# Optimization experiments

Hardware: AMD Instinct MI355X
Metric: run time of the kernel (lower is better)

The kernel has to match this reference:

```python
import jax, jax.numpy as jnp
import numpy as np

N_NODES = 50000
N_EDGES = 800000
IN_HID = 64
OUT_HID = 64
EXT_DIM = 32


def setup_inputs() -> dict:
    key = jax.random.key(0)
    ks = jax.random.split(key, 9)
    h = jax.random.normal(ks[0], (N_NODES, IN_HID), dtype=jnp.float32)
    e_h = jax.random.normal(ks[1], (N_EDGES, IN_HID), dtype=jnp.float32)
    ext_feature = jax.random.normal(ks[2], (N_EDGES, EXT_DIM), dtype=jnp.float32)
    # fc1: Linear(3*in_hid -> in_hid); fc2: Linear(in_hid+ext_dim -> out_hid)
    W1 = jax.random.normal(ks[3], (3 * IN_HID, IN_HID), dtype=jnp.float32) * 0.05
    b1 = jax.random.normal(ks[4], (IN_HID,), dtype=jnp.float32) * 0.05
    W2 = jax.random.normal(ks[5], (IN_HID + EXT_DIM, OUT_HID), dtype=jnp.float32) * 0.05
    b2 = jax.random.normal(ks[6], (OUT_HID,), dtype=jnp.float32) * 0.05
    src = jax.random.randint(ks[7], (N_EDGES,), 0, N_NODES, dtype=jnp.int64 if jax.config.jax_enable_x64 else jnp.int32)
    dst = jax.random.randint(ks[8], (N_EDGES,), 0, N_NODES, dtype=jnp.int64 if jax.config.jax_enable_x64 else jnp.int32)
    return {"h": h, "e_h": e_h, "ext_feature": ext_feature,
            "W1": W1, "b1": b1, "W2": W2, "b2": b2,
            "src": src, "dst": dst}


def reference(h, e_h, ext_feature, W1, b1, W2, b2, src, dst):
    # apply_edge: gather src/dst node features, concat with edge feature
    evt = jnp.concatenate([h[src], e_h, h[dst]], axis=-1)          # [E, 3*in_hid]
    x = evt @ W1 + b1                                              # fc1 (dropout=0 -> identity)
    x = jnp.concatenate([x, ext_feature], axis=-1)                 # [E, in_hid+ext_dim]
    out = jax.nn.relu(x @ W2 + b2)                                 # fc2 + relu; activation=None
    return out                                                     # new edge feature e_h [E, out_hid]
```

## Files before the change

### kernel.cpp

```cpp
#include <hip/hip_runtime.h>


typedef __attribute__((ext_vector_type(8))) short bf16x8;
typedef __attribute__((ext_vector_type(4))) float f32x4;

__device__ __forceinline__ short f2bf(float f) {
  unsigned u = __builtin_bit_cast(unsigned, f);
  u = (u + 0x7FFFu + ((u >> 16) & 1u)) >> 16;
  return (short)u;
}


__global__ __launch_bounds__(256, 2) void edge_mp_kernel(
    const float* __restrict__ h, const float* __restrict__ e_h,
    const float* __restrict__ ext, const float* __restrict__ W1,
    const float* __restrict__ b1, const float* __restrict__ W2,
    const float* __restrict__ b2, const int* __restrict__ src,
    const int* __restrict__ dst, float* __restrict__ out, int E) {
  __shared__ __align__(16) short lds[30720];
  const int tid = threadIdx.x;
  const int l = tid & 63;
  const int wid = tid >> 6;
  const int i = l & 15;
  const int q = l >> 4;
  const int i2 = l >> 2;
  const int c = l & 3;

  for (int s = tid; s < 1536; s += 256) {
    int kc = s >> 8, nt = (s >> 6) & 3, ll = s & 63;
    int k0 = kc * 32 + ((ll >> 4) * 8), n = nt * 16 + (ll & 15);
#pragma unroll
    for (int j = 0; j < 8; ++j) lds[s * 8 + j] = f2bf(W1[(k0 + j) * 64 + n]);
  }
  for (int s = tid; s < 768; s += 256) {
    int kc = s >> 8, nt = (s >> 6) & 3, ll = s & 63;
    int k0 = kc * 32 + ((ll >> 4) * 8), n = nt * 16 + (ll & 15);
#pragma unroll
    for (int j = 0; j < 8; ++j)
      lds[12288 + s * 8 + j] = f2bf(W2[(k0 + j) * 64 + n]);
  }
  __syncthreads();

  float b1v[4], b2v[4];
#pragma unroll
  for (int nt = 0; nt < 4; ++nt) {
    b1v[nt] = b1[nt * 16 + i];
    b2v[nt] = b2[nt * 16 + i];
  }

  short* evt = &lds[18432 + wid * 3072];

  for (int it = 0; it < 4; ++it) {
    const int e0 = blockIdx.x * 256 + it * 64 + wid * 16;
    if (e0 >= E) break;
    int e = e0 + i2;
    if (e >= E) e = E - 1;
    const int sI = src[e], dI = dst[e];
    const float* srcp[3] = {h + (size_t)sI * 64, e_h + (size_t)e * 64,
                            h + (size_t)dI * 64};

#pragma unroll
    for (int s = 0; s < 3; ++s) {
#pragma unroll
      for (int t = 0; t < 4; ++t) {
        const int k0 = 16 * t + 4 * c;
        float4 v = *(const float4*)(srcp[s] + k0);
        const int kc = s * 2 + (t >> 1);
        const int quad = 2 * (t & 1) + (c >> 1);
        const int j0 = 4 * (c & 1);
        short4 p;
        p.x = f2bf(v.x); p.y = f2bf(v.y); p.z = f2bf(v.z); p.w = f2bf(v.w);
        *(short4*)&evt[(kc * 64 + quad * 16 + i2) * 8 + j0] = p;
      }
    }

    f32x4 acc[4] = {{0.f, 0.f, 0.f, 0.f},
                    {0.f, 0.f, 0.f, 0.f},
                    {0.f, 0.f, 0.f, 0.f},
                    {0.f, 0.f, 0.f, 0.f}};
#pragma unroll
    for (int kc = 0; kc < 6; ++kc) {
      bf16x8 a = *(const bf16x8*)&evt[(kc * 64 + l) * 8];
#pragma unroll
      for (int nt = 0; nt < 4; ++nt) {
        bf16x8 b = *(const bf16x8*)&lds[((kc * 4 + nt) * 64 + l) * 8];
        acc[nt] = __builtin_amdgcn_mfma_f32_16x16x32_bf16(a, b, acc[nt], 0, 0, 0);
      }
    }

#pragma unroll
    for (int nt = 0; nt < 4; ++nt) {
      const int n = nt * 16 + i;
      const int kc2 = n >> 5, qA = (n & 31) >> 3, j = n & 7;
#pragma unroll
      for (int r = 0; r < 4; ++r) {
        const int m = q * 4 + r;
        evt[(kc2 * 64 + qA * 16 + m) * 8 + j] = f2bf(acc[nt][r] + b1v[nt]);
      }
    }
#pragma unroll
    for (int t = 0; t < 2; ++t) {
      float4 v = *(const float4*)(ext + (size_t)e * 32 + 16 * t + 4 * c);
      const int quad = 2 * t + (c >> 1);
      const int j0 = 4 * (c & 1);
      short4 p;
      p.x = f2bf(v.x); p.y = f2bf(v.y); p.z = f2bf(v.z); p.w = f2bf(v.w);
      *(short4*)&evt[(2 * 64 + quad * 16 + i2) * 8 + j0] = p;
    }

    f32x4 acc2[4] = {{0.f, 0.f, 0.f, 0.f},
                     {0.f, 0.f, 0.f, 0.f},
                     {0.f, 0.f, 0.f, 0.f},
                     {0.f, 0.f, 0.f, 0.f}};
#pragma unroll
    for (int kc = 0; kc < 3; ++kc) {
      bf16x8 a = *(const bf16x8*)&evt[(kc * 64 + l) * 8];
#pragma unroll
      for (int nt = 0; nt < 4; ++nt) {
        bf16x8 b = *(const bf16x8*)&lds[12288 + ((kc * 4 + nt) * 64 + l) * 8];
        acc2[nt] =
            __builtin_amdgcn_mfma_f32_16x16x32_bf16(a, b, acc2[nt], 0, 0, 0);
      }
    }

#pragma unroll
    for (int nt = 0; nt < 4; ++nt) {
      const int n = nt * 16 + i;
#pragma unroll
      for (int r = 0; r < 4; ++r) {
        const int er = e0 + q * 4 + r;
        if (er < E) {
          float v = acc2[nt][r] + b2v[nt];
          out[(size_t)er * 64 + n] = fmaxf(v, 0.f);
        }
      }
    }
  }
}

extern "C" void kernel_launch(void* const* d_in, const int* in_sizes, int n_in,
                              void* d_out, int out_size, void* d_ws,
                              size_t ws_size, hipStream_t stream) {
  const float* h = (const float*)d_in[0];
  const float* e_h = (const float*)d_in[1];
  const float* ext = (const float*)d_in[2];
  const float* W1 = (const float*)d_in[3];
  const float* b1 = (const float*)d_in[4];
  const float* W2 = (const float*)d_in[5];
  const float* b2 = (const float*)d_in[6];
  const int* src = (const int*)d_in[7];
  const int* dst = (const int*)d_in[8];
  float* out = (float*)d_out;
  const int E = in_sizes[7];
  const int blocks = (E + 255) / 256;
  hipLaunchKernelGGL(edge_mp_kernel, dim3(blocks), dim3(256), 0, stream, h, e_h,
                     ext, W1, b1, W2, b2, src, dst, out, E);
}
```

Before: 457.4 us.

## Load gathered features straight into MFMA A registers and prefetch edge indices

The fc1 A operand is now built directly in registers. Each lane loads the 16-row by 32-k slice that matches the MFMA operand layout from the src, edge and dst feature rows, so the per-wave LDS staging buffer for the 192-wide concat is gone and only the fc2 input is staged. Next iteration's src/dst indices are prefetched and the ext loads are issued early to hide gather latency. Blocks grow to 512 threads with launch_bounds(512,4). That launch bound squeezes registers against the twelve float4 held per lane, which risks spilling or lower occupancy.

```diff
diff --git a/kernel.cpp b/kernel.cpp
--- a/kernel.cpp
+++ b/kernel.cpp
@@ -3,6 +3,7 @@
 
 typedef __attribute__((ext_vector_type(8))) short bf16x8;
 typedef __attribute__((ext_vector_type(4))) float f32x4;
+typedef __attribute__((ext_vector_type(4))) short s16x4;
 
 __device__ __forceinline__ short f2bf(float f) {
   unsigned u = __builtin_bit_cast(unsigned, f);
@@ -10,8 +11,10 @@
   return (short)u;
 }
 
+#define ITERS 4
 
-__global__ __launch_bounds__(256, 2) void edge_mp_kernel(
+
+__global__ __launch_bounds__(512, 4) void edge_mp_kernel(
     const float* __restrict__ h, const float* __restrict__ e_h,
     const float* __restrict__ ext, const float* __restrict__ W1,
     const float* __restrict__ b1, const float* __restrict__ W2,
@@ -26,13 +29,13 @@
   const int i2 = l >> 2;
   const int c = l & 3;
 
-  for (int s = tid; s < 1536; s += 256) {
+  for (int s = tid; s < 1536; s += 512) {
     int kc = s >> 8, nt = (s >> 6) & 3, ll = s & 63;
     int k0 = kc * 32 + ((ll >> 4) * 8), n = nt * 16 + (ll & 15);
 #pragma unroll
     for (int j = 0; j < 8; ++j) lds[s * 8 + j] = f2bf(W1[(k0 + j) * 64 + n]);
   }
-  for (int s = tid; s < 768; s += 256) {
+  for (int s = tid; s < 768; s += 512) {
     int kc = s >> 8, nt = (s >> 6) & 3, ll = s & 63;
     int k0 = kc * 32 + ((ll >> 4) * 8), n = nt * 16 + (ll & 15);
 #pragma unroll
@@ -48,29 +51,54 @@
     b2v[nt] = b2[nt * 16 + i];
   }
 
-  short* evt = &lds[18432 + wid * 3072];
+  short* xw = &lds[18432 + wid * 1536];
 
-  for (int it = 0; it < 4; ++it) {
-    const int e0 = blockIdx.x * 256 + it * 64 + wid * 16;
+  const int base = blockIdx.x * (128 * ITERS) + wid * 16;
+
+  int nS = 0, nD = 0;
+  if (base < E) {
+    int e = base + i;
+    if (e >= E) e = E - 1;
+    nS = src[e];
+    nD = dst[e];
+  }
+
+#pragma unroll 1
+  for (int it = 0; it < ITERS; ++it) {
+    const int e0 = base + it * 128;
     if (e0 >= E) break;
-    int e = e0 + i2;
+    int e = e0 + i;
     if (e >= E) e = E - 1;
-    const int sI = src[e], dI = dst[e];
-    const float* srcp[3] = {h + (size_t)sI * 64, e_h + (size_t)e * 64,
-                            h + (size_t)dI * 64};
 
-#pragma unroll
-    for (int s = 0; s < 3; ++s) {
-#pragma unroll
-      for (int t = 0; t < 4; ++t) {
-        const int k0 = 16 * t + 4 * c;
-        float4 v = *(const float4*)(srcp[s] + k0);
-        const int kc = s * 2 + (t >> 1);
-        const int quad = 2 * (t & 1) + (c >> 1);
-        const int j0 = 4 * (c & 1);
-        short4 p;
-        p.x = f2bf(v.x); p.y = f2bf(v.y); p.z = f2bf(v.z); p.w = f2bf(v.w);
-        *(short4*)&evt[(kc * 64 + quad * 16 + i2) * 8 + j0] = p;
+    const float* ps = h + (size_t)nS * 64 + q * 8;
+    const float* pe = e_h + (size_t)e * 64 + q * 8;
+    const float* pd = h + (size_t)nD * 64 + q * 8;
+    f32x4 L[12];
+    L[0] = *(const f32x4*)(ps);
+    L[1] = *(const f32x4*)(ps + 4);
+    L[2] = *(const f32x4*)(ps + 32);
+    L[3] = *(const f32x4*)(ps + 36);
+    L[4] = *(const f32x4*)(pe);
+    L[5] = *(const f32x4*)(pe + 4);
+    L[6] = *(const f32x4*)(pe + 32);
+    L[7] = *(const f32x4*)(pe + 36);
+    L[8] = *(const f32x4*)(pd);
+    L[9] = *(const f32x4*)(pd + 4);
+    L[10] = *(const f32x4*)(pd + 32);
+    L[11] = *(const f32x4*)(pd + 36);
+
+    int ex = e0 + i2;
+    if (ex >= E) ex = E - 1;
+    f32x4 X0 = *(const f32x4*)(ext + (size_t)ex * 32 + 4 * c);
+    f32x4 X1 = *(const f32x4*)(ext + (size_t)ex * 32 + 16 + 4 * c);
+
+    if (it + 1 < ITERS) {
+      const int en0 = e0 + 128;
+      if (en0 < E) {
+        int en = en0 + i;
+        if (en >= E) en = E - 1;
+        nS = src[en];
+        nD = dst[en];
       }
     }
 
@@ -80,7 +108,12 @@
                     {0.f, 0.f, 0.f, 0.f}};
 #pragma unroll
     for (int kc = 0; kc < 6; ++kc) {
-      bf16x8 a = *(const bf16x8*)&evt[(kc * 64 + l) * 8];
+      bf16x8 a;
+#pragma unroll
+      for (int j = 0; j < 4; ++j) {
+        a[j] = f2bf(L[2 * kc][j]);
+        a[4 + j] = f2bf(L[2 * kc + 1][j]);
+      }
 #pragma unroll
       for (int nt = 0; nt < 4; ++nt) {
         bf16x8 b = *(const bf16x8*)&lds[((kc * 4 + nt) * 64 + l) * 8];
@@ -95,17 +128,20 @@
 #pragma unroll
       for (int r = 0; r < 4; ++r) {
         const int m = q * 4 + r;
-        evt[(kc2 * 64 + qA * 16 + m) * 8 + j] = f2bf(acc[nt][r] + b1v[nt]);
+        xw[(kc2 * 64 + qA * 16 + m) * 8 + j] = f2bf(acc[nt][r] + b1v[nt]);
       }
     }
 #pragma unroll
     for (int t = 0; t < 2; ++t) {
-      float4 v = *(const float4*)(ext + (size_t)e * 32 + 16 * t + 4 * c);
+      f32x4 v = t ? X1 : X0;
       const int quad = 2 * t + (c >> 1);
       const int j0 = 4 * (c & 1);
-      short4 p;
-      p.x = f2bf(v.x); p.y = f2bf(v.y); p.z = f2bf(v.z); p.w = f2bf(v.w);
-      *(short4*)&evt[(2 * 64 + quad * 16 + i2) * 8 + j0] = p;
+      s16x4 p;
+      p[0] = f2bf(v[0]);
+      p[1] = f2bf(v[1]);
+      p[2] = f2bf(v[2]);
+      p[3] = f2bf(v[3]);
+      *(s16x4*)&xw[(2 * 64 + quad * 16 + i2) * 8 + j0] = p;
     }
 
     f32x4 acc2[4] = {{0.f, 0.f, 0.f, 0.f},
@@ -114,7 +150,7 @@
                      {0.f, 0.f, 0.f, 0.f}};
 #pragma unroll
     for (int kc = 0; kc < 3; ++kc) {
-      bf16x8 a = *(const bf16x8*)&evt[(kc * 64 + l) * 8];
+      bf16x8 a = *(const bf16x8*)&xw[(kc * 64 + l) * 8];
 #pragma unroll
       for (int nt = 0; nt < 4; ++nt) {
         bf16x8 b = *(const bf16x8*)&lds[12288 + ((kc * 4 + nt) * 64 + l) * 8];
@@ -152,7 +188,7 @@
   const int* dst = (const int*)d_in[8];
   float* out = (float*)d_out;
   const int E = in_sizes[7];
-  const int blocks = (E + 255) / 256;
-  hipLaunchKernelGGL(edge_mp_kernel, dim3(blocks), dim3(256), 0, stream, h, e_h,
+  const int blocks = (E + (128 * ITERS) - 1) / (128 * ITERS);
+  hipLaunchKernelGGL(edge_mp_kernel, dim3(blocks), dim3(512), 0, stream, h, e_h,
                      ext, W1, b1, W2, b2, src, dst, out, E);
 }
```

After: 463.1 us. No clear change (+1.2%).
